# Kernel optimization log

Measured on AMD Instinct MI355X. Metric: run time of the kernel, lower is better.

The kernel has to match this reference:

```python
import jax, jax.numpy as jnp
import numpy as np

N_NODES = 100000
N_EDGES = 4000000
CHANNELS = 64


def setup_inputs() -> dict:
    key = jax.random.key(0)
    k1, k2, k3, k4, k5 = jax.random.split(key, 5)
    x = jax.random.normal(k1, (N_NODES, CHANNELS), dtype=jnp.float32)
    sources = jax.random.randint(k2, (N_EDGES,), 0, N_NODES, dtype=jnp.int64)
    targets = jax.random.randint(k3, (N_EDGES,), 0, N_NODES, dtype=jnp.int64)
    norm = jax.random.uniform(k4, (N_NODES, 1), dtype=jnp.float32)
    # xavier_normal_ for a (64, 64) weight: std = sqrt(2 / (fan_in + fan_out))
    std = float(np.sqrt(2.0 / (CHANNELS + CHANNELS)))
    weight = jax.random.normal(k5, (CHANNELS, CHANNELS), dtype=jnp.float32) * std
    return {"x": x, "sources": sources, "targets": targets, "norm": norm, "weight": weight}


def reference(x, sources, targets, norm, weight):
    # x.index_add(0, targets, x[sources]) == x + segment_sum(x[sources], targets)
    messages = x[sources]  # [E, C] gather
    agg = x + jax.ops.segment_sum(messages, targets, num_segments=x.shape[0])  # [N, C]
    h = norm * agg  # per-node scale, norm broadcasts [N,1] over [N,C]
    return h @ weight  # [N, C]
```

## Files before the change

### kernel.cpp

```cpp
#include <hip/hip_runtime.h>


constexpr int C = 64;
constexpr int BN = 128;
constexpr int CHUNK2 = 8192;
constexpr int MAXB = 1024;
constexpr int CAP = 6144;

__global__ __launch_bounds__(512) void prep_kernel(
    const float* __restrict__ x, unsigned* __restrict__ xb,
    const int* __restrict__ tgt, int* __restrict__ bhist,
    int E, int NB, int histBlocks, int total8) {
  __shared__ int h[MAXB];
  if ((int)blockIdx.x < histBlocks) {
    for (int i = threadIdx.x; i < NB; i += 512) h[i] = 0;
    __syncthreads();
    int base = blockIdx.x * CHUNK2;
    int end = base + CHUNK2; if (end > E) end = E;
    for (int i = base + threadIdx.x; i < end; i += 512)
      atomicAdd(&h[tgt[i] >> 7], 1);
    __syncthreads();
    for (int i = threadIdx.x; i < NB; i += 512)
      if (h[i]) atomicAdd(&bhist[i], h[i]);
  } else {
    int i = (blockIdx.x - histBlocks) * 512 + threadIdx.x;
    if (i < total8) {
      const float4* x4 = (const float4*)x;
      float4 a = x4[i * 2], bq = x4[i * 2 + 1];
      float f[8] = {a.x, a.y, a.z, a.w, bq.x, bq.y, bq.z, bq.w};
      unsigned w[4];
#pragma unroll
      for (int k = 0; k < 4; k++) {
        unsigned u0 = __float_as_uint(f[2 * k]);
        unsigned u1 = __float_as_uint(f[2 * k + 1]);
        u0 = (u0 + 0x7FFFu + ((u0 >> 16) & 1u)) >> 16;
        u1 = (u1 + 0x7FFFu + ((u1 >> 16) & 1u)) >> 16;
        w[k] = u0 | (u1 << 16);
      }
      ((uint4*)xb)[i] = make_uint4(w[0], w[1], w[2], w[3]);
    }
  }
}

__global__ __launch_bounds__(256) void bscan_kernel(
    const int* __restrict__ bhist, int* __restrict__ bbase,
    int* __restrict__ cursor, int NB) {
  __shared__ int partials[256];
  int tid = threadIdx.x;
  int per = (NB + 255) / 256;
  int lo = tid * per, hi = lo + per;
  if (lo > NB) lo = NB;
  if (hi > NB) hi = NB;
  int s = 0;
  for (int i = lo; i < hi; i++) s += bhist[i];
  partials[tid] = s;
  __syncthreads();
  for (int off = 1; off < 256; off <<= 1) {
    int v = partials[tid];
    int a = (tid >= off) ? partials[tid - off] : 0;
    __syncthreads();
    partials[tid] = v + a;
    __syncthreads();
  }
  int run = partials[tid] - s;
  for (int i = lo; i < hi; i++) { bbase[i] = run; cursor[i] = run; run += bhist[i]; }
  if (tid == 255) bbase[NB] = partials[255];
}

__global__ __launch_bounds__(512) void bin_kernel(
    const int* __restrict__ src, const int* __restrict__ tgt,
    int* __restrict__ gcursor, unsigned* __restrict__ recs, int E, int NB) {
  __shared__ unsigned rec[CHUNK2];
  __shared__ unsigned short bkt[CHUNK2];
  __shared__ int hist[MAXB];
  __shared__ int gb[MAXB];
  int tid = threadIdx.x;
  int base = blockIdx.x * CHUNK2;
  int count = E - base; if (count > CHUNK2) count = CHUNK2;

  for (int i = tid; i < NB; i += 512) hist[i] = 0;
  __syncthreads();
  for (int i = tid; i < count; i += 512) {
    int s = src[base + i], t = tgt[base + i];
    int b = t >> 7;
    rec[i] = ((unsigned)s << 7) | (unsigned)(t & 127);
    bkt[i] = (unsigned short)b;
    atomicAdd(&hist[b], 1);
  }
  __syncthreads();
  for (int i = tid; i < NB; i += 512) {
    int c = hist[i];
    gb[i] = c ? atomicAdd(&gcursor[i], c) : 0;
  }
  __syncthreads();
  for (int i = tid; i < NB; i += 512) hist[i] = 0;
  __syncthreads();
  for (int i = tid; i < count; i += 512) {
    int b = (int)bkt[i];
    int idx = atomicAdd(&hist[b], 1);
    recs[gb[b] + idx] = rec[i];
  }
}

template <bool USE_BF16>
__global__ __launch_bounds__(512) void sortgather_kernel(
    const float* __restrict__ x, const unsigned* __restrict__ xb,
    const unsigned* __restrict__ recs, const int* __restrict__ bbase,
    const float* __restrict__ norm, const float* __restrict__ W,
    float* __restrict__ out, int N) {
  __shared__ int cnt[BN];
  __shared__ int pre[BN];
  __shared__ int nstart[BN + 1];
  __shared__ int sorted[CAP];
  int tid = threadIdx.x;
  int lane = tid & 63;
  int wave = tid >> 6;
  int b = blockIdx.x;
  int n0 = b * BN;
  int nn = N - n0; if (nn > BN) nn = BN;
  int beg = bbase[b], end = bbase[b + 1];
  int m = end - beg;

  float wreg[C];
#pragma unroll
  for (int k = 0; k < C; k++) wreg[k] = W[k * C + lane];

  if (tid < BN) cnt[tid] = 0;
  __syncthreads();
  for (int r = beg + tid; r < end; r += 512)
    atomicAdd(&cnt[recs[r] & 127u], 1);
  __syncthreads();
  if (tid < BN) pre[tid] = cnt[tid];
  __syncthreads();
  for (int off = 1; off < BN; off <<= 1) {
    int v = 0, a = 0;
    if (tid < BN) { v = pre[tid]; a = (tid >= off) ? pre[tid - off] : 0; }
    __syncthreads();
    if (tid < BN) pre[tid] = v + a;
    __syncthreads();
  }
  if (tid < BN) {
    nstart[tid] = pre[tid] - cnt[tid];
    cnt[tid] = pre[tid] - cnt[tid];
  }
  if (tid == 0) nstart[BN] = m;
  __syncthreads();
  bool fits = (m <= CAP);
  if (fits) {
    for (int r = beg + tid; r < end; r += 512) {
      unsigned rc = recs[r];
      int p = atomicAdd(&cnt[rc & 127u], 1);
      sorted[p] = (int)(rc >> 7);
    }
  }
  __syncthreads();

  int sub, grp;
  if (USE_BF16) { sub = lane & 7;  grp = lane >> 3; }
  else          { sub = lane & 15; grp = lane >> 4; }
  const float4* x4 = (const float4*)x;
  const uint4* xb4 = (const uint4*)xb;

  for (int i = wave; i < nn; i += 8) {
    int n = n0 + i;
    float acc[8];
    if (grp == 0) {
      if (USE_BF16) {
        float4 a = x4[n * 16 + sub * 2], bq = x4[n * 16 + sub * 2 + 1];
        acc[0] = a.x; acc[1] = a.y; acc[2] = a.z; acc[3] = a.w;
        acc[4] = bq.x; acc[5] = bq.y; acc[6] = bq.z; acc[7] = bq.w;
      } else {
        float4 a = x4[n * 16 + sub];
        acc[0] = a.x; acc[1] = a.y; acc[2] = a.z; acc[3] = a.w;
        acc[4] = acc[5] = acc[6] = acc[7] = 0.0f;
      }
    } else {
#pragma unroll
      for (int j = 0; j < 8; j++) acc[j] = 0.0f;
    }

    if (fits) {
      int gbeg = nstart[i], gend = nstart[i + 1];
      if (USE_BF16) {
        for (int e0 = gbeg; e0 < gend; e0 += 64) {
#pragma unroll
          for (int u = 0; u < 8; u++) {
            int e = e0 + 8 * u + grp;
            if (e < gend) {
              int s = sorted[e];
              uint4 v = xb4[s * 8 + sub];
              acc[0] += __uint_as_float(v.x << 16);
              acc[1] += __uint_as_float(v.x & 0xFFFF0000u);
              acc[2] += __uint_as_float(v.y << 16);
              acc[3] += __uint_as_float(v.y & 0xFFFF0000u);
              acc[4] += __uint_as_float(v.z << 16);
              acc[5] += __uint_as_float(v.z & 0xFFFF0000u);
              acc[6] += __uint_as_float(v.w << 16);
              acc[7] += __uint_as_float(v.w & 0xFFFF0000u);
            }
          }
        }
      } else {
        for (int e0 = gbeg; e0 < gend; e0 += 16) {
#pragma unroll
          for (int u = 0; u < 4; u++) {
            int e = e0 + 4 * u + grp;
            if (e < gend) {
              int s = sorted[e];
              float4 v = x4[s * 16 + sub];
              acc[0] += v.x; acc[1] += v.y; acc[2] += v.z; acc[3] += v.w;
            }
          }
        }
      }
    } else {
      for (int r0 = beg; r0 < end; r0 += (USE_BF16 ? 8 : 4)) {
        int e = r0 + grp;
        if (e < end) {
          unsigned rc = recs[e];
          if ((int)(rc & 127u) == i) {
            int s = (int)(rc >> 7);
            if (USE_BF16) {
              uint4 v = xb4[s * 8 + sub];
              acc[0] += __uint_as_float(v.x << 16);
              acc[1] += __uint_as_float(v.x & 0xFFFF0000u);
              acc[2] += __uint_as_float(v.y << 16);
              acc[3] += __uint_as_float(v.y & 0xFFFF0000u);
              acc[4] += __uint_as_float(v.z << 16);
              acc[5] += __uint_as_float(v.z & 0xFFFF0000u);
              acc[6] += __uint_as_float(v.w << 16);
              acc[7] += __uint_as_float(v.w & 0xFFFF0000u);
            } else {
              float4 v = x4[s * 16 + sub];
              acc[0] += v.x; acc[1] += v.y; acc[2] += v.z; acc[3] += v.w;
            }
          }
        }
      }
    }

    if (USE_BF16) {
#pragma unroll
      for (int j = 0; j < 8; j++) {
        acc[j] += __shfl_xor(acc[j], 8, 64);
        acc[j] += __shfl_xor(acc[j], 16, 64);
        acc[j] += __shfl_xor(acc[j], 32, 64);
      }
    } else {
#pragma unroll
      for (int j = 0; j < 4; j++) {
        acc[j] += __shfl_xor(acc[j], 16, 64);
        acc[j] += __shfl_xor(acc[j], 32, 64);
      }
    }

    float nv = norm[n];
    float o = 0.0f;
    if (USE_BF16) {
#pragma unroll
      for (int j = 0; j < 8; j++) acc[j] *= nv;
#pragma unroll
      for (int s = 0; s < 8; s++)
#pragma unroll
        for (int j = 0; j < 8; j++)
          o = fmaf(__shfl(acc[j], s, 64), wreg[8 * s + j], o);
    } else {
#pragma unroll
      for (int j = 0; j < 4; j++) acc[j] *= nv;
#pragma unroll
      for (int s = 0; s < 16; s++)
#pragma unroll
        for (int j = 0; j < 4; j++)
          o = fmaf(__shfl(acc[j], s, 64), wreg[4 * s + j], o);
    }
    out[n * C + lane] = o;
  }
}

extern "C" void kernel_launch(void* const* d_in, const int* in_sizes, int n_in,
                              void* d_out, int out_size, void* d_ws, size_t ws_size,
                              hipStream_t stream) {
  const float* x       = (const float*)d_in[0];
  const int*   sources = (const int*)d_in[1];
  const int*   targets = (const int*)d_in[2];
  const float* norm    = (const float*)d_in[3];
  const float* weight  = (const float*)d_in[4];
  float* out = (float*)d_out;

  int N = in_sizes[0] / C;
  int E = in_sizes[1];
  int NB = (N + BN - 1) / BN;

  size_t xb_words = (size_t)N * C / 2;
  size_t meta_words = (size_t)3 * NB + 1 + (size_t)E;
  bool use_bf16 = ws_size >= (xb_words + meta_words) * 4;

  unsigned* xb; int* bhist;
  if (use_bf16) {
    xb = (unsigned*)d_ws;
    bhist = (int*)d_ws + xb_words;
  } else {
    xb = nullptr;
    bhist = (int*)d_ws;
  }
  int* bbase  = bhist + NB;
  int* cursor = bbase + (NB + 1);
  unsigned* recs = (unsigned*)(cursor + NB);

  hipMemsetAsync(bhist, 0, (size_t)NB * sizeof(int), stream);

  int hb = (E + CHUNK2 - 1) / CHUNK2;
  int total8 = N * C / 8;
  int cvtBlocks = use_bf16 ? (total8 + 511) / 512 : 0;
  prep_kernel<<<hb + cvtBlocks, 512, 0, stream>>>(x, xb, targets, bhist, E, NB, hb, total8);
  bscan_kernel<<<1, 256, 0, stream>>>(bhist, bbase, cursor, NB);
  bin_kernel<<<hb, 512, 0, stream>>>(sources, targets, cursor, recs, E, NB);
  if (use_bf16) {
    sortgather_kernel<true><<<NB, 512, 0, stream>>>(x, xb, recs, bbase, norm, weight, out, N);
  } else {
    sortgather_kernel<false><<<NB, 512, 0, stream>>>(x, xb, recs, bbase, norm, weight, out, N);
  }
}
```

Baseline: 311.8 us.

## Split per-node gather into source-range passes with shared-memory accumulators

Each node's edges are now bucketed by target node and by a coarse source-index range (three ranges taken from high record bits), and the gather runs in three passes. Every pass only touches one slice of source rows across the block, which is meant to improve L2 locality of the random gathers. Partial sums go into a padded shared-memory accumulator seeded with x, and a final loop applies the weight matmul and the norm. This adds about 33KB of shared memory and more syncs and scan work, uses shorter unrolls per node, and sets launch bounds to 4 blocks per CU, which may cap registers and cost occupancy.

```diff
diff --git a/kernel.cpp b/kernel.cpp
--- a/kernel.cpp
+++ b/kernel.cpp
@@ -6,6 +6,9 @@
 constexpr int CHUNK2 = 8192;
 constexpr int MAXB = 1024;
 constexpr int CAP = 6144;
+constexpr int NPASS = 3;
+constexpr int BINS = BN * 4;
+constexpr int ASTRIDE = 65;
 
 __global__ __launch_bounds__(512) void prep_kernel(
     const float* __restrict__ x, unsigned* __restrict__ xb,
@@ -103,15 +106,16 @@
 }
 
 template <bool USE_BF16>
-__global__ __launch_bounds__(512) void sortgather_kernel(
+__global__ __launch_bounds__(512, 4) void sortgather_kernel(
     const float* __restrict__ x, const unsigned* __restrict__ xb,
     const unsigned* __restrict__ recs, const int* __restrict__ bbase,
     const float* __restrict__ norm, const float* __restrict__ W,
     float* __restrict__ out, int N) {
-  __shared__ int cnt[BN];
-  __shared__ int pre[BN];
-  __shared__ int nstart[BN + 1];
-  __shared__ int sorted[CAP];
+  __shared__ int cnt[BINS];
+  __shared__ int pre[BINS];
+  __shared__ int nst[BINS + 1];
+  __shared__ unsigned sorted[CAP];
+  __shared__ float accum[BN * ASTRIDE];
   int tid = threadIdx.x;
   int lane = tid & 63;
   int wave = tid >> 6;
@@ -125,32 +129,42 @@
 #pragma unroll
   for (int k = 0; k < C; k++) wreg[k] = W[k * C + lane];
 
-  if (tid < BN) cnt[tid] = 0;
-  __syncthreads();
-  for (int r = beg + tid; r < end; r += 512)
-    atomicAdd(&cnt[recs[r] & 127u], 1);
-  __syncthreads();
-  if (tid < BN) pre[tid] = cnt[tid];
-  __syncthreads();
-  for (int off = 1; off < BN; off <<= 1) {
-    int v = 0, a = 0;
-    if (tid < BN) { v = pre[tid]; a = (tid >= off) ? pre[tid - off] : 0; }
-    __syncthreads();
-    if (tid < BN) pre[tid] = v + a;
-    __syncthreads();
-  }
-  if (tid < BN) {
-    nstart[tid] = pre[tid] - cnt[tid];
-    cnt[tid] = pre[tid] - cnt[tid];
-  }
-  if (tid == 0) nstart[BN] = m;
+  for (int i = tid; i < nn * C; i += 512) {
+    int node = i >> 6, c = i & 63;
+    accum[node * ASTRIDE + c] = x[(n0 + node) * C + c];
+  }
+
+  cnt[tid] = 0;
+  __syncthreads();
+  for (int r = beg + tid; r < end; r += 512) {
+    unsigned rc = recs[r];
+    int q = (int)(rc >> 22); if (q > 2) q = 2;
+    atomicAdd(&cnt[(int)(rc & 127u) * 4 + q], 1);
+  }
+  __syncthreads();
+  pre[tid] = cnt[tid];
+  __syncthreads();
+  for (int off = 1; off < BINS; off <<= 1) {
+    int v = pre[tid];
+    int a = (tid >= off) ? pre[tid - off] : 0;
+    __syncthreads();
+    pre[tid] = v + a;
+    __syncthreads();
+  }
+  {
+    int excl = pre[tid] - cnt[tid];
+    nst[tid] = excl;
+    cnt[tid] = excl;
+  }
+  if (tid == 0) nst[BINS] = m;
   __syncthreads();
   bool fits = (m <= CAP);
   if (fits) {
     for (int r = beg + tid; r < end; r += 512) {
       unsigned rc = recs[r];
-      int p = atomicAdd(&cnt[rc & 127u], 1);
-      sorted[p] = (int)(rc >> 7);
+      int q = (int)(rc >> 22); if (q > 2) q = 2;
+      int p = atomicAdd(&cnt[(int)(rc & 127u) * 4 + q], 1);
+      sorted[p] = rc >> 7;
     }
   }
   __syncthreads();
@@ -161,33 +175,84 @@
   const float4* x4 = (const float4*)x;
   const uint4* xb4 = (const uint4*)xb;
 
-  for (int i = wave; i < nn; i += 8) {
-    int n = n0 + i;
-    float acc[8];
-    if (grp == 0) {
+  if (fits) {
+    for (int p = 0; p < NPASS; p++) {
+      for (int i = wave; i < nn; i += 8) {
+        int gbeg = nst[i * 4 + p], gend = nst[i * 4 + p + 1];
+        if (gbeg == gend) continue;
+        if (USE_BF16) {
+          float acc[8];
+#pragma unroll
+          for (int j = 0; j < 8; j++) acc[j] = 0.0f;
+          for (int e0 = gbeg; e0 < gend; e0 += 16) {
+#pragma unroll
+            for (int u = 0; u < 2; u++) {
+              int e = e0 + 8 * u + grp;
+              if (e < gend) {
+                int s = (int)sorted[e];
+                uint4 v = xb4[s * 8 + sub];
+                acc[0] += __uint_as_float(v.x << 16);
+                acc[1] += __uint_as_float(v.x & 0xFFFF0000u);
+                acc[2] += __uint_as_float(v.y << 16);
+                acc[3] += __uint_as_float(v.y & 0xFFFF0000u);
+                acc[4] += __uint_as_float(v.z << 16);
+                acc[5] += __uint_as_float(v.z & 0xFFFF0000u);
+                acc[6] += __uint_as_float(v.w << 16);
+                acc[7] += __uint_as_float(v.w & 0xFFFF0000u);
+              }
+            }
+          }
+#pragma unroll
+          for (int j = 0; j < 8; j++) {
+            acc[j] += __shfl_xor(acc[j], 8, 64);
+            acc[j] += __shfl_xor(acc[j], 16, 64);
+            acc[j] += __shfl_xor(acc[j], 32, 64);
+          }
+          float v = acc[0];
+#pragma unroll
+          for (int j = 1; j < 8; j++) v = (grp == j) ? acc[j] : v;
+          int c = sub * 8 + grp;
+          accum[i * ASTRIDE + c] += v;
+        } else {
+          float acc[4];
+#pragma unroll
+          for (int j = 0; j < 4; j++) acc[j] = 0.0f;
+          for (int e0 = gbeg; e0 < gend; e0 += 8) {
+#pragma unroll
+            for (int u = 0; u < 2; u++) {
+              int e = e0 + 4 * u + grp;
+              if (e < gend) {
+                int s = (int)sorted[e];
+                float4 v = x4[s * 16 + sub];
+                acc[0] += v.x; acc[1] += v.y; acc[2] += v.z; acc[3] += v.w;
+              }
+            }
+          }
+#pragma unroll
+          for (int j = 0; j < 4; j++) {
+            acc[j] += __shfl_xor(acc[j], 16, 64);
+            acc[j] += __shfl_xor(acc[j], 32, 64);
+          }
+          float v = acc[0];
+#pragma unroll
+          for (int j = 1; j < 4; j++) v = ((grp & 3) == j) ? acc[j] : v;
+          int c = sub * 4 + (grp & 3);
+          accum[i * ASTRIDE + c] += v;
+        }
+      }
+    }
+  } else {
+    for (int i = wave; i < nn; i += 8) {
       if (USE_BF16) {
-        float4 a = x4[n * 16 + sub * 2], bq = x4[n * 16 + sub * 2 + 1];
-        acc[0] = a.x; acc[1] = a.y; acc[2] = a.z; acc[3] = a.w;
-        acc[4] = bq.x; acc[5] = bq.y; acc[6] = bq.z; acc[7] = bq.w;
-      } else {
-        float4 a = x4[n * 16 + sub];
-        acc[0] = a.x; acc[1] = a.y; acc[2] = a.z; acc[3] = a.w;
-        acc[4] = acc[5] = acc[6] = acc[7] = 0.0f;
-      }
-    } else {
-#pragma unroll
-      for (int j = 0; j < 8; j++) acc[j] = 0.0f;
-    }
-
-    if (fits) {
-      int gbeg = nstart[i], gend = nstart[i + 1];
-      if (USE_BF16) {
-        for (int e0 = gbeg; e0 < gend; e0 += 64) {
-#pragma unroll
-          for (int u = 0; u < 8; u++) {
-            int e = e0 + 8 * u + grp;
-            if (e < gend) {
-              int s = sorted[e];
+        float acc[8];
+#pragma unroll
+        for (int j = 0; j < 8; j++) acc[j] = 0.0f;
+        for (int r0 = beg; r0 < end; r0 += 8) {
+          int e = r0 + grp;
+          if (e < end) {
+            unsigned rc = recs[e];
+            if ((int)(rc & 127u) == i) {
+              int s = (int)(rc >> 7);
               uint4 v = xb4[s * 8 + sub];
               acc[0] += __uint_as_float(v.x << 16);
               acc[1] += __uint_as_float(v.x & 0xFFFF0000u);
@@ -200,80 +265,53 @@
             }
           }
         }
+#pragma unroll
+        for (int j = 0; j < 8; j++) {
+          acc[j] += __shfl_xor(acc[j], 8, 64);
+          acc[j] += __shfl_xor(acc[j], 16, 64);
+          acc[j] += __shfl_xor(acc[j], 32, 64);
+        }
+        float v = acc[0];
+#pragma unroll
+        for (int j = 1; j < 8; j++) v = (grp == j) ? acc[j] : v;
+        accum[i * ASTRIDE + sub * 8 + grp] += v;
       } else {
-        for (int e0 = gbeg; e0 < gend; e0 += 16) {
-#pragma unroll
-          for (int u = 0; u < 4; u++) {
-            int e = e0 + 4 * u + grp;
-            if (e < gend) {
-              int s = sorted[e];
+        float acc[4];
+#pragma unroll
+        for (int j = 0; j < 4; j++) acc[j] = 0.0f;
+        for (int r0 = beg; r0 < end; r0 += 4) {
+          int e = r0 + grp;
+          if (e < end) {
+            unsigned rc = recs[e];
+            if ((int)(rc & 127u) == i) {
+              int s = (int)(rc >> 7);
               float4 v = x4[s * 16 + sub];
               acc[0] += v.x; acc[1] += v.y; acc[2] += v.z; acc[3] += v.w;
             }
           }
         }
-      }
-    } else {
-      for (int r0 = beg; r0 < end; r0 += (USE_BF16 ? 8 : 4)) {
-        int e = r0 + grp;
-        if (e < end) {
-          unsigned rc = recs[e];
-          if ((int)(rc & 127u) == i) {
-            int s = (int)(rc >> 7);
-            if (USE_BF16) {
-              uint4 v = xb4[s * 8 + sub];
-              acc[0] += __uint_as_float(v.x << 16);
-              acc[1] += __uint_as_float(v.x & 0xFFFF0000u);
-              acc[2] += __uint_as_float(v.y << 16);
-              acc[3] += __uint_as_float(v.y & 0xFFFF0000u);
-              acc[4] += __uint_as_float(v.z << 16);
-              acc[5] += __uint_as_float(v.z & 0xFFFF0000u);
-              acc[6] += __uint_as_float(v.w << 16);
-              acc[7] += __uint_as_float(v.w & 0xFFFF0000u);
-            } else {
-              float4 v = x4[s * 16 + sub];
-              acc[0] += v.x; acc[1] += v.y; acc[2] += v.z; acc[3] += v.w;
-            }
-          }
-        }
+#pragma unroll
+        for (int j = 0; j < 4; j++) {
+          acc[j] += __shfl_xor(acc[j], 16, 64);
+          acc[j] += __shfl_xor(acc[j], 32, 64);
+        }
+        float v = acc[0];
+#pragma unroll
+        for (int j = 1; j < 4; j++) v = ((grp & 3) == j) ? acc[j] : v;
+        accum[i * ASTRIDE + sub * 4 + (grp & 3)] += v;
       }
     }
-
-    if (USE_BF16) {
-#pragma unroll
-      for (int j = 0; j < 8; j++) {
-        acc[j] += __shfl_xor(acc[j], 8, 64);
-        acc[j] += __shfl_xor(acc[j], 16, 64);
-        acc[j] += __shfl_xor(acc[j], 32, 64);
-      }
-    } else {
-#pragma unroll
-      for (int j = 0; j < 4; j++) {
-        acc[j] += __shfl_xor(acc[j], 16, 64);
-        acc[j] += __shfl_xor(acc[j], 32, 64);
-      }
-    }
-
-    float nv = norm[n];
+  }
+  __syncthreads();
+
+  for (int i = wave; i < nn; i += 8) {
+    int n = n0 + i;
+    float a = accum[i * ASTRIDE + lane];
     float o = 0.0f;
-    if (USE_BF16) {
-#pragma unroll
-      for (int j = 0; j < 8; j++) acc[j] *= nv;
-#pragma unroll
-      for (int s = 0; s < 8; s++)
-#pragma unroll
-        for (int j = 0; j < 8; j++)
-          o = fmaf(__shfl(acc[j], s, 64), wreg[8 * s + j], o);
-    } else {
-#pragma unroll
-      for (int j = 0; j < 4; j++) acc[j] *= nv;
-#pragma unroll
-      for (int s = 0; s < 16; s++)
-#pragma unroll
-        for (int j = 0; j < 4; j++)
-          o = fmaf(__shfl(acc[j], s, 64), wreg[4 * s + j], o);
-    }
-    out[n * C + lane] = o;
+#pragma unroll
+    for (int c = 0; c < C; c++)
+      o = fmaf(__shfl(a, c, 64), wreg[c], o);
+    out[n * C + lane] = o * norm[n];
   }
 }
 
```

Result: slower. 392.7 us (+26.0%).
